# Kernel optimization log

Measured on AMD Instinct MI355X. Metric: run time of the kernel, lower is better.

## Reference

```python
import jax, jax.numpy as jnp
import numpy as np

D_MODEL = 1024
NGRAM = 2
SHIFT_STEP = 1


def induction_head(ids, hidden, ngram=NGRAM, shift_step=SHIFT_STEP):
    # ids: [B, S] int, hidden: [B, S, D]
    B, S = ids.shape
    eq = ids[:, None, :] == ids[:, :, None]                      # [B, S, S]
    causal = jnp.tril(jnp.ones((S, S), dtype=bool), k=-1)        # strictly lower
    m = jnp.logical_and(eq, causal)
    acc = m
    cur = m
    for _ in range(1, ngram):
        # F.pad(cur, (1,-1,1,-1)): shift down-right by 1 on the [S,S] dims
        cur = jnp.pad(cur, ((0, 0), (1, 0), (1, 0)))[:, :S, :S]
        acc = jnp.logical_and(acc, cur)                          # stack+sum>=ngram == AND
    ih = acc
    if shift_step > 0:
        # F.pad(ih, (shift,-shift)): shift right by shift_step on last dim
        ih = jnp.pad(ih, ((0, 0), (0, 0), (shift_step, 0)))[:, :, :S]
    ih = jnp.logical_and(ih, causal)
    ihf = ih.astype(hidden.dtype)
    denom = jnp.sum(ihf, axis=2, keepdims=True)
    norm = jnp.where(denom > 0, ihf / jnp.where(denom > 0, denom, 1), 0)  # nan_to_num(0)
    return jnp.einsum('bmn,bnz->bmz', norm, hidden)


def setup_inputs() -> dict:
    key = jax.random.key(0)
    k1, k2, k3, k4, k5, k6 = jax.random.split(key, 6)
    B, S, D = 4, 2048, D_MODEL
    x = jax.random.normal(k1, (B, S, D), dtype=jnp.float32)
    input_ids = jax.random.randint(k2, (B, S), 0, 512, dtype=jnp.int64)
    s = 1.0 / np.sqrt(D)
    W0 = jax.random.uniform(k3, (D, D), jnp.float32, -s, s)
    b0 = jax.random.uniform(k4, (D,), jnp.float32, -s, s)
    W1 = jax.random.uniform(k5, (D, D), jnp.float32, -s, s)
    b1 = jax.random.uniform(k6, (D,), jnp.float32, -s, s)
    return {"x": x, "input_ids": input_ids, "W0": W0, "b0": b0, "W1": W1, "b1": b1}


def reference(x, input_ids, W0, b0, W1, b1):
    h0 = induction_head(input_ids, x, ngram=NGRAM)
    h1 = x
    y = h0 @ W0.T + b0 + (h1 @ W1.T + b1)
    return y
```

## Files before the change

### kernel.cpp

```cpp
#include <hip/hip_runtime.h>
#include <hip/hip_bf16.h>

#define BATCH   4
#define S_LEN   2048
#define DMODEL  1024
#define M_TOT   (BATCH * S_LEN)
#define N_TOT   DMODEL
#define K_TOT   DMODEL

#define MAXR    2048
#define RSLOTS  256

#define CNT_OFF   0
#define ROWS_OFF  1024
#define AVG_OFF   16384
#define XBF_OFF   (10u * 1024u * 1024u)
#define WBF_OFF   (27u * 1024u * 1024u)
#define FULL_NEED (30u * 1024u * 1024u)
#define MID_NEED  (9u * 1024u * 1024u)

typedef __attribute__((ext_vector_type(8))) short bf16x8;
typedef __attribute__((ext_vector_type(4))) short bf16x4v;
typedef __attribute__((ext_vector_type(4))) float f32x4;

__device__ __forceinline__ short f2bf(float f) {
  union { float f; unsigned int u; } v; v.f = f;
  unsigned int u = v.u;
  u += 0x7fffu + ((u >> 16) & 1u);
  return (short)(u >> 16);
}

#define GLOAD(gp, lp)                                               \
  __builtin_amdgcn_global_load_lds(                                 \
      (const __attribute__((address_space(1))) void*)(gp),          \
      (__attribute__((address_space(3))) void*)(lp), 16, 0, 0)

__global__ void init_kernel(int* __restrict__ cnt) {
  if (threadIdx.x == 0) *cnt = 0;
}

#define NX8 (M_TOT * K_TOT / 8)
#define NW8 (N_TOT * K_TOT / 8)
__global__ __launch_bounds__(256) void cvt2_kernel(
    const float* __restrict__ x, short* __restrict__ xo,
    const float* __restrict__ w, short* __restrict__ wo) {
  int idx = blockIdx.x * 256 + threadIdx.x;
  const float* in; short* out; int k;
  if (idx < NX8)             { in = x; out = xo; k = idx; }
  else if (idx < NX8 + NW8)  { in = w; out = wo; k = idx - NX8; }
  else return;
  const float4* p = (const float4*)in + (size_t)k * 2;
  float4 a = p[0], b = p[1];
  bf16x8 v = { f2bf(a.x), f2bf(a.y), f2bf(a.z), f2bf(a.w),
               f2bf(b.x), f2bf(b.y), f2bf(b.z), f2bf(b.w) };
  *(bf16x8*)(out + (size_t)k * 8) = v;
}

__global__ __launch_bounds__(256) void gemm_bf16_kernel(
    const short* __restrict__ Ab, const short* __restrict__ Bb,
    const float* __restrict__ b0, const float* __restrict__ b1,
    float* __restrict__ C) {
  __shared__ short As[2][128 * 32];
  __shared__ short Bs[2][128 * 32];

  const int tid  = threadIdx.x;
  const int lane = tid & 63;
  const int w    = tid >> 6;
  const int wm   = w >> 1, wn = w & 1;

  const int swz = (blockIdx.x & 7) * 64 + (blockIdx.x >> 3);
  const int bn  = swz & 7, bm = swz >> 3;

  const int l15 = lane & 15;
  const int kc  = (lane >> 4) << 3;

  const short* Abase = Ab + (size_t)bm * 128 * K_TOT;
  const short* Bbase = Bb + (size_t)bn * 128 * K_TOT;

  const int srow = tid >> 2;
  const int scol = (tid & 3) << 3;
  const int lbase = (tid & ~63) * 8;

  f32x4 acc[4][4];
#pragma unroll
  for (int a = 0; a < 4; a++)
#pragma unroll
    for (int b = 0; b < 4; b++) {
      f32x4 z = {0.f, 0.f, 0.f, 0.f};
      acc[a][b] = z;
    }

#define STG(buf, k0)                                                        \
  {                                                                         \
    _Pragma("unroll")                                                       \
    for (int q = 0; q < 2; ++q) {                                           \
      GLOAD(Abase + (size_t)(q * 64 + srow) * K_TOT + (k0) + scol,          \
            &As[buf][q * 2048 + lbase]);                                    \
      GLOAD(Bbase + (size_t)(q * 64 + srow) * K_TOT + (k0) + scol,          \
            &Bs[buf][q * 2048 + lbase]);                                    \
    }                                                                       \
  }

  STG(0, 0);
  __syncthreads();

  const int NT = K_TOT / 32;
  for (int t = 0; t < NT; ++t) {
    const int cur = t & 1;
    if (t + 1 < NT) STG(cur ^ 1, (t + 1) * 32);

    bf16x8 af[4], bb[4];
#pragma unroll
    for (int mi = 0; mi < 4; ++mi)
      af[mi] = *(const bf16x8*)&As[cur][(wm * 64 + mi * 16 + l15) * 32 + kc];
#pragma unroll
    for (int ni = 0; ni < 4; ++ni)
      bb[ni] = *(const bf16x8*)&Bs[cur][(wn * 64 + ni * 16 + l15) * 32 + kc];

#pragma unroll
    for (int mi = 0; mi < 4; ++mi)
#pragma unroll
      for (int ni = 0; ni < 4; ++ni)
        acc[mi][ni] = __builtin_amdgcn_mfma_f32_16x16x32_bf16(
            af[mi], bb[ni], acc[mi][ni], 0, 0, 0);

    __syncthreads();
  }
#undef STG

#pragma unroll
  for (int ni = 0; ni < 4; ni++) {
    const int col = bn * 128 + wn * 64 + ni * 16 + l15;
    const float bias = b0[col] + b1[col];
#pragma unroll
    for (int mi = 0; mi < 4; mi++) {
      const int row0 = bm * 128 + wm * 64 + mi * 16 + ((lane >> 4) << 2);
#pragma unroll
      for (int r = 0; r < 4; r++)
        C[(size_t)(row0 + r) * N_TOT + col] = acc[mi][ni][r] + bias;
    }
  }
}

#define BM 128
#define BN 128
#define BK 32
#define LDK 40

__global__ __launch_bounds__(256) void gemm_bias_kernel(
    const float* __restrict__ A, const float* __restrict__ Bw,
    const float* __restrict__ b0, const float* __restrict__ b1,
    float* __restrict__ C) {
  __shared__ short As[2][BM][LDK];
  __shared__ short Bs[2][BM][LDK];

  const int tid  = threadIdx.x;
  const int lane = tid & 63;
  const int w    = tid >> 6;
  const int wm   = w >> 1, wn = w & 1;
  const int bn   = blockIdx.x & 7;
  const int bm   = blockIdx.x >> 3;
  const int l15 = lane & 15;
  const int kc  = (lane >> 4) << 3;

  f32x4 acc[4][4];
#pragma unroll
  for (int a = 0; a < 4; a++)
#pragma unroll
    for (int b = 0; b < 4; b++) {
      f32x4 z = {0.f, 0.f, 0.f, 0.f};
      acc[a][b] = z;
    }

  const float* Abase = A  + (size_t)bm * BM * K_TOT;
  const float* Bbase = Bw + (size_t)bn * BN * K_TOT;
  float4 ra[4], rb[4];

#define LOADT(k0)                                                          \
  {                                                                        \
    _Pragma("unroll")                                                      \
    for (int q = 0; q < 4; q++) {                                          \
      int fidx = tid + q * 256;                                            \
      int r = fidx >> 3, cc = (fidx & 7) << 2;                             \
      ra[q] = *(const float4*)(Abase + (size_t)r * K_TOT + (k0) + cc);     \
      rb[q] = *(const float4*)(Bbase + (size_t)r * K_TOT + (k0) + cc);     \
    }                                                                      \
  }
#define STORET(buf)                                                        \
  {                                                                        \
    _Pragma("unroll")                                                      \
    for (int q = 0; q < 4; q++) {                                          \
      int fidx = tid + q * 256;                                            \
      int r = fidx >> 3, cc = (fidx & 7) << 2;                             \
      bf16x4v av = { f2bf(ra[q].x), f2bf(ra[q].y),                         \
                     f2bf(ra[q].z), f2bf(ra[q].w) };                       \
      bf16x4v bv = { f2bf(rb[q].x), f2bf(rb[q].y),                         \
                     f2bf(rb[q].z), f2bf(rb[q].w) };                       \
      *(bf16x4v*)&As[buf][r][cc] = av;                                     \
      *(bf16x4v*)&Bs[buf][r][cc] = bv;                                     \
    }                                                                      \
  }

  LOADT(0);
  STORET(0);
  __syncthreads();

  const int NT = K_TOT / BK;
  for (int t = 0; t < NT; ++t) {
    const int cur = t & 1;
    if (t + 1 < NT) LOADT((t + 1) * BK);
    bf16x8 af[4], bf_[4];
#pragma unroll
    for (int mi = 0; mi < 4; mi++)
      af[mi] = *(const bf16x8*)&As[cur][wm * 64 + mi * 16 + l15][kc];
#pragma unroll
    for (int ni = 0; ni < 4; ni++)
      bf_[ni] = *(const bf16x8*)&Bs[cur][wn * 64 + ni * 16 + l15][kc];
#pragma unroll
    for (int mi = 0; mi < 4; mi++)
#pragma unroll
      for (int ni = 0; ni < 4; ni++)
        acc[mi][ni] = __builtin_amdgcn_mfma_f32_16x16x32_bf16(
            af[mi], bf_[ni], acc[mi][ni], 0, 0, 0);
    if (t + 1 < NT) STORET(cur ^ 1);
    __syncthreads();
  }
#undef LOADT
#undef STORET

#pragma unroll
  for (int ni = 0; ni < 4; ni++) {
    const int col = bn * BN + wn * 64 + ni * 16 + l15;
    const float bias = b0[col] + b1[col];
#pragma unroll
    for (int mi = 0; mi < 4; mi++) {
      const int row0 = bm * BM + wm * 64 + mi * 16 + ((lane >> 4) << 2);
#pragma unroll
      for (int r = 0; r < 4; r++)
        C[(size_t)(row0 + r) * N_TOT + col] = acc[mi][ni][r] + bias;
    }
  }
}

__global__ __launch_bounds__(256) void matchscan_kernel(
    const int* __restrict__ ids, int* __restrict__ cnt,
    int* __restrict__ rows) {
  const int blk = blockIdx.x;
  const int b   = blk >> 6;
  const int r0  = (blk & 63) * 32;
  __shared__ int s_ids[S_LEN];
  __shared__ __align__(16) int keys[S_LEN];
  const int tid = threadIdx.x;

#pragma unroll
  for (int h = 0; h < 8; ++h)
    s_ids[tid + h * 256] = ids[b * S_LEN + tid + h * 256];
  __syncthreads();
#pragma unroll
  for (int h = 0; h < 8; ++h) {
    int i = tid + h * 256;
    keys[i] = (i > 0) ? (s_ids[i - 1] * 512 + s_ids[i]) : -1;
  }
  __syncthreads();

  const int row = r0 + (tid >> 3);
  const int sl  = tid & 7;
  int c = 0;
  if (row >= 3) {
    const int ki   = keys[row];
    const int pmax = row - 2;
    const int4* k4 = (const int4*)keys;
    for (int q = sl; q * 4 <= pmax; q += 8) {
      int4 kk = k4[q];
      int p0 = q * 4;
      c += (p0     >= 1 && p0     <= pmax && kk.x == ki);
      c += (p0 + 1 <= pmax && kk.y == ki);
      c += (p0 + 2 <= pmax && kk.z == ki);
      c += (p0 + 3 <= pmax && kk.w == ki);
    }
  }
  c += __shfl_down(c, 1, 8);
  c += __shfl_down(c, 2, 8);
  c += __shfl_down(c, 4, 8);
  if (sl == 0 && row >= 3 && c > 0) {
    int slot = atomicAdd(cnt, 1);
    if (slot < MAXR) rows[slot] = b * S_LEN + row;
  }
}

__global__ __launch_bounds__(256) void gather_kernel(
    const int* __restrict__ cnt, const int* __restrict__ rows,
    const int* __restrict__ ids, const float* __restrict__ x,
    float* __restrict__ avg) {
  int R = *cnt; if (R > MAXR) R = MAXR;
  const int tid = threadIdx.x;
  __shared__ int s_cnt;
  __shared__ int s_list[S_LEN];
  __shared__ int s_keys[S_LEN];
  int cur_b = -1;

  for (int slot = blockIdx.x; slot < R; slot += RSLOTS) {
    const int row = rows[slot];
    const int b = row >> 11, i = row & (S_LEN - 1);
    if (b != cur_b) {
      __syncthreads();
      const int* idb = ids + b * S_LEN;
#pragma unroll
      for (int h = 0; h < 8; ++h) {
        int p = tid + h * 256;
        int idp  = idb[p];
        int idpm = (p > 0) ? idb[p - 1] : -2;
        s_keys[p] = (p > 0) ? (idpm * 512 + idp) : -1;
      }
      cur_b = b;
    }
    if (tid == 0) s_cnt = 0;
    __syncthreads();

    const int ki = s_keys[i];
    for (int p = 1 + tid; p <= i - 2; p += 256)
      if (s_keys[p] == ki) { int q = atomicAdd(&s_cnt, 1); s_list[q] = p + 1; }
    __syncthreads();

    const int c = s_cnt;
    float4 s = {0.f, 0.f, 0.f, 0.f};
    const float4* xb = (const float4*)(x + (size_t)b * S_LEN * DMODEL);
    for (int r = 0; r < c; ++r) {
      const int j = s_list[r];
      float4 v = xb[(size_t)j * (DMODEL / 4) + tid];
      s.x += v.x; s.y += v.y; s.z += v.z; s.w += v.w;
    }
    const float inv = 1.0f / (float)c;
    s.x *= inv; s.y *= inv; s.z *= inv; s.w *= inv;
    *(float4*)(avg + (size_t)slot * DMODEL + tid * 4) = s;
    __syncthreads();
  }
}

__global__ __launch_bounds__(256) void apply_kernel(
    const int* __restrict__ cnt, const int* __restrict__ rows,
    const float* __restrict__ avg, const float* __restrict__ W0,
    float* __restrict__ y) {
  int R = *cnt; if (R > MAXR) R = MAXR;
  const int rslot = blockIdx.x >> 4;
  if (rslot >= R) return;
  const int cg = blockIdx.x & 15;
  const int tid = threadIdx.x;

  __shared__ float s_avg[DMODEL];

  for (int r = rslot; r < R; r += RSLOTS) {
    if (r != rslot) __syncthreads();
    *(float4*)&s_avg[tid * 4] =
        *(const float4*)(avg + (size_t)r * DMODEL + tid * 4);
    __syncthreads();

    const int n  = cg * 64 + (tid >> 2);
    const int ks = (tid & 3) * 256;
    const float4* wr = (const float4*)(W0 + (size_t)n * DMODEL + ks);
    const float4* ar = (const float4*)&s_avg[ks];
    float a = 0.f;
#pragma unroll 8
    for (int u = 0; u < 64; ++u) {
      float4 wv = wr[u], av = ar[u];
      a += wv.x * av.x + wv.y * av.y + wv.z * av.z + wv.w * av.w;
    }
    a += __shfl_down(a, 1, 4);
    a += __shfl_down(a, 2, 4);
    if ((tid & 3) == 0) {
      const int m = rows[r];
      y[(size_t)m * DMODEL + n] += a;
    }
  }
}

__global__ __launch_bounds__(256) void induct_kernel(
    const int* __restrict__ ids, const float* __restrict__ x,
    const float* __restrict__ W0, float* __restrict__ y) {
  const int b = blockIdx.x >> 11;
  const int i = blockIdx.x & (S_LEN - 1);
  if (i < 3) return;
  const int* idb = ids + b * S_LEN;
  __shared__ int   s_cnt;
  __shared__ int   s_list[S_LEN];
  __shared__ float s_avg[DMODEL];
  const int tid = threadIdx.x;
  if (tid == 0) s_cnt = 0;
  __syncthreads();
  const int ti = idb[i], tp = idb[i - 1];
  for (int j = 2 + tid; j < i; j += 256) {
    if (idb[j - 1] == ti && idb[j - 2] == tp) {
      int p = atomicAdd(&s_cnt, 1);
      s_list[p] = j;
    }
  }
  __syncthreads();
  const int c = s_cnt;
  if (c == 0) return;
  float4 s = {0.f, 0.f, 0.f, 0.f};
  const float4* xb = (const float4*)(x + (size_t)b * S_LEN * DMODEL);
  for (int r = 0; r < c; ++r) {
    const int j = s_list[r];
    float4 v = xb[(size_t)j * (DMODEL / 4) + tid];
    s.x += v.x; s.y += v.y; s.z += v.z; s.w += v.w;
  }
  const float inv = 1.0f / (float)c;
  s.x *= inv; s.y *= inv; s.z *= inv; s.w *= inv;
  *(float4*)&s_avg[tid * 4] = s;
  __syncthreads();
  float out[4];
#pragma unroll
  for (int q = 0; q < 4; ++q) {
    const int n = q * 256 + tid;
    const float4* wr = (const float4*)(W0 + (size_t)n * DMODEL);
    float a = 0.f;
    for (int kk = 0; kk < DMODEL / 4; ++kk) {
      float4 wv = wr[kk];
      float4 av = *(const float4*)&s_avg[kk * 4];
      a += wv.x * av.x + wv.y * av.y + wv.z * av.z + wv.w * av.w;
    }
    out[q] = a;
  }
  float* yrow = y + ((size_t)(b * S_LEN + i)) * DMODEL;
#pragma unroll
  for (int q = 0; q < 4; ++q) yrow[q * 256 + tid] += out[q];
}

extern "C" void kernel_launch(void* const* d_in, const int* in_sizes, int n_in,
                              void* d_out, int out_size, void* d_ws, size_t ws_size,
                              hipStream_t stream) {
  const float* x   = (const float*)d_in[0];
  const int*   ids = (const int*)  d_in[1];
  const float* W0  = (const float*)d_in[2];
  const float* b0  = (const float*)d_in[3];
  const float* W1  = (const float*)d_in[4];
  const float* b1  = (const float*)d_in[5];
  float* y = (float*)d_out;

  char* ws = (char*)d_ws;
  int*   cnt  = (int*)(ws + CNT_OFF);
  int*   rows = (int*)(ws + ROWS_OFF);
  float* avg  = (float*)(ws + AVG_OFF);
  short* xbf  = (short*)(ws + XBF_OFF);
  short* wbf  = (short*)(ws + WBF_OFF);

  const bool full = ws_size >= FULL_NEED;
  const bool mid  = ws_size >= MID_NEED;

  if (mid) {
    init_kernel<<<1, 64, 0, stream>>>(cnt);
    matchscan_kernel<<<BATCH * 64, 256, 0, stream>>>(ids, cnt, rows);
    gather_kernel<<<RSLOTS, 256, 0, stream>>>(cnt, rows, ids, x, avg);
  }

  if (full) {
    cvt2_kernel<<<(NX8 + NW8 + 255) / 256, 256, 0, stream>>>(x, xbf, W1, wbf);
    gemm_bf16_kernel<<<(M_TOT / 128) * (N_TOT / 128), 256, 0, stream>>>(xbf, wbf, b0, b1, y);
  } else {
    gemm_bias_kernel<<<(M_TOT / BM) * (N_TOT / BN), 256, 0, stream>>>(x, W1, b0, b1, y);
  }

  if (mid) {
    apply_kernel<<<RSLOTS * 16, 256, 0, stream>>>(cnt, rows, avg, W0, y);
  } else {
    induct_kernel<<<BATCH * S_LEN, 256, 0, stream>>>(ids, x, W0, y);
  }
}
```

Baseline: 149.8 us.

## Keep W0 rows in registers in apply kernel and fold counter init into convert

The apply kernel is restructured so each wave owns one output column and holds that column's W0 row in registers. It then streams batches of 16 averaged rows through shared memory, so W0 is read once per block instead of once per matched row. The separate counter-init launch is removed by zeroing the counter inside the conversion kernel, which saves one launch in the full-workspace path. The cost is a full 64-lane shuffle reduction per row and a serial loop over all matched rows in every block, with only 256 blocks launched.

```diff
diff --git a/kernel.cpp b/kernel.cpp
--- a/kernel.cpp
+++ b/kernel.cpp
@@ -43,8 +43,10 @@
 #define NW8 (N_TOT * K_TOT / 8)
 __global__ __launch_bounds__(256) void cvt2_kernel(
     const float* __restrict__ x, short* __restrict__ xo,
-    const float* __restrict__ w, short* __restrict__ wo) {
+    const float* __restrict__ w, short* __restrict__ wo,
+    int* __restrict__ cnt) {
   int idx = blockIdx.x * 256 + threadIdx.x;
+  if (idx == 0) *cnt = 0;
   const float* in; short* out; int k;
   if (idx < NX8)             { in = x; out = xo; k = idx; }
   else if (idx < NX8 + NW8)  { in = w; out = wo; k = idx - NX8; }
@@ -342,35 +344,45 @@
     const float* __restrict__ avg, const float* __restrict__ W0,
     float* __restrict__ y) {
   int R = *cnt; if (R > MAXR) R = MAXR;
-  const int rslot = blockIdx.x >> 4;
-  if (rslot >= R) return;
-  const int cg = blockIdx.x & 15;
+  if (R == 0) return;
   const int tid = threadIdx.x;
-
-  __shared__ float s_avg[DMODEL];
-
-  for (int r = rslot; r < R; r += RSLOTS) {
-    if (r != rslot) __syncthreads();
-    *(float4*)&s_avg[tid * 4] =
-        *(const float4*)(avg + (size_t)r * DMODEL + tid * 4);
-    __syncthreads();
-
-    const int n  = cg * 64 + (tid >> 2);
-    const int ks = (tid & 3) * 256;
-    const float4* wr = (const float4*)(W0 + (size_t)n * DMODEL + ks);
-    const float4* ar = (const float4*)&s_avg[ks];
-    float a = 0.f;
-#pragma unroll 8
-    for (int u = 0; u < 64; ++u) {
-      float4 wv = wr[u], av = ar[u];
-      a += wv.x * av.x + wv.y * av.y + wv.z * av.z + wv.w * av.w;
-    }
-    a += __shfl_down(a, 1, 4);
-    a += __shfl_down(a, 2, 4);
-    if ((tid & 3) == 0) {
-      const int m = rows[r];
-      y[(size_t)m * DMODEL + n] += a;
-    }
+  const int c   = tid >> 6;
+  const int ks  = tid & 63;
+  const int n   = blockIdx.x * 4 + c;
+
+  const float4* wr = (const float4*)(W0 + (size_t)n * DMODEL);
+  float4 w0 = wr[ks], w1 = wr[ks + 64], w2 = wr[ks + 128], w3 = wr[ks + 192];
+
+  __shared__ float4 s_avg[16][256];
+
+  for (int r0 = 0; r0 < R; r0 += 16) {
+    const int nch = min(16, R - r0);
+    {
+      const int rr = tid >> 4, fp = tid & 15;
+      if (rr < nch) {
+        const float4* ar = (const float4*)(avg + (size_t)(r0 + rr) * DMODEL);
+#pragma unroll
+        for (int u = 0; u < 16; ++u)
+          s_avg[rr][fp + 16 * u] = ar[fp + 16 * u];
+      }
+    }
+    __syncthreads();
+
+    for (int rr = 0; rr < nch; ++rr) {
+      float4 a0 = s_avg[rr][ks], a1 = s_avg[rr][ks + 64],
+             a2 = s_avg[rr][ks + 128], a3 = s_avg[rr][ks + 192];
+      float a = w0.x * a0.x + w0.y * a0.y + w0.z * a0.z + w0.w * a0.w
+              + w1.x * a1.x + w1.y * a1.y + w1.z * a1.z + w1.w * a1.w
+              + w2.x * a2.x + w2.y * a2.y + w2.z * a2.z + w2.w * a2.w
+              + w3.x * a3.x + w3.y * a3.y + w3.z * a3.z + w3.w * a3.w;
+#pragma unroll
+      for (int s = 32; s >= 1; s >>= 1) a += __shfl_down(a, s, 64);
+      if (ks == 0) {
+        const int m = rows[r0 + rr];
+        y[(size_t)m * DMODEL + n] += a;
+      }
+    }
+    __syncthreads();
   }
 }
 
@@ -447,22 +459,20 @@
   const bool full = ws_size >= FULL_NEED;
   const bool mid  = ws_size >= MID_NEED;
 
-  if (mid) {
+  if (full) {
+    cvt2_kernel<<<(NX8 + NW8 + 255) / 256, 256, 0, stream>>>(x, xbf, W1, wbf, cnt);
+    matchscan_kernel<<<BATCH * 64, 256, 0, stream>>>(ids, cnt, rows);
+    gather_kernel<<<RSLOTS, 256, 0, stream>>>(cnt, rows, ids, x, avg);
+    gemm_bf16_kernel<<<(M_TOT / 128) * (N_TOT / 128), 256, 0, stream>>>(xbf, wbf, b0, b1, y);
+    apply_kernel<<<256, 256, 0, stream>>>(cnt, rows, avg, W0, y);
+  } else if (mid) {
     init_kernel<<<1, 64, 0, stream>>>(cnt);
     matchscan_kernel<<<BATCH * 64, 256, 0, stream>>>(ids, cnt, rows);
     gather_kernel<<<RSLOTS, 256, 0, stream>>>(cnt, rows, ids, x, avg);
-  }
-
-  if (full) {
-    cvt2_kernel<<<(NX8 + NW8 + 255) / 256, 256, 0, stream>>>(x, xbf, W1, wbf);
-    gemm_bf16_kernel<<<(M_TOT / 128) * (N_TOT / 128), 256, 0, stream>>>(xbf, wbf, b0, b1, y);
+    gemm_bias_kernel<<<(M_TOT / BM) * (N_TOT / BN), 256, 0, stream>>>(x, W1, b0, b1, y);
+    apply_kernel<<<256, 256, 0, stream>>>(cnt, rows, avg, W0, y);
   } else {
     gemm_bias_kernel<<<(M_TOT / BM) * (N_TOT / BN), 256, 0, stream>>>(x, W1, b0, b1, y);
-  }
-
-  if (mid) {
-    apply_kernel<<<RSLOTS * 16, 256, 0, stream>>>(cnt, rows, avg, W0, y);
-  } else {
     induct_kernel<<<BATCH * S_LEN, 256, 0, stream>>>(ids, x, W0, y);
   }
 }
```

After: 155.1 us. 1.04x slower.
